# Optimization experiments

Measured on AMD Instinct MI355X. Metric: run time of the kernel, lower is better.

## Reference

```python
import jax, jax.numpy as jnp
import numpy as np

B, T, K, D = 32, 512, 4, 256
E, M = 100000, 2048
NEG = -10000000000.0


def setup_inputs() -> dict:
    key = jax.random.key(0)
    ks = jax.random.split(key, 8)
    token_reprs = jax.random.normal(ks[0], (B, T, K, D), dtype=jnp.float32)
    edge_index = jax.random.randint(ks[1], (2, E), 0, B * T, dtype=jnp.int64)
    lm_indices = jax.random.randint(ks[2], (M,), 0, B * T * K, dtype=jnp.int64)
    batch_pointers = jax.random.randint(ks[3], (M,), 0, B, dtype=jnp.int64)
    tree_padding_mask = jax.random.bernoulli(ks[4], 0.8, (B, T))
    # SwiGLU(2*dim, 4*dim, 1) parameters (no biases)
    sg = 1.0 / np.sqrt(2 * D)
    sh = 1.0 / np.sqrt(4 * D)
    Wg = jax.random.normal(ks[5], (2 * D, 4 * D), dtype=jnp.float32) * sg
    Wv = jax.random.normal(ks[6], (2 * D, 4 * D), dtype=jnp.float32) * sg
    Wo = jax.random.normal(ks[7], (4 * D, 1), dtype=jnp.float32) * sh
    return {
        "token_reprs": token_reprs,
        "Wg": Wg,
        "Wv": Wv,
        "Wo": Wo,
        "edge_index": edge_index,
        "lm_indices": lm_indices,
        "batch_pointers": batch_pointers,
        "tree_padding_mask": tree_padding_mask,
    }


def reference(token_reprs, Wg, Wv, Wo, edge_index, lm_indices, batch_pointers, tree_padding_mask):
    b, t, k, d = token_reprs.shape
    # predict_lemmas: gather type reprs via edge_index, concat, SwiGLU MLP
    type_flat = token_reprs[:, :, 0].reshape(b * t, d)           # [B*T, D]
    scope_ids, goal_ids = edge_index[0], edge_index[1]
    x = jnp.concatenate([type_flat[scope_ids], type_flat[goal_ids]], axis=-1)  # [E, 2D]
    h = jax.nn.silu(x @ Wg) * (x @ Wv)                           # [E, 4D]
    lemmas = (h @ Wo).squeeze(-1)                                # [E]
    # predict_masks: gathers + masked dot-product scoring
    mask_reprs = token_reprs.reshape(-1, d)[lm_indices]          # [M, D]
    type_reprs = token_reprs[:, :, 0]                            # [B, T, D]
    candidates = type_reprs[batch_pointers]                      # [M, T, D]
    candidate_mask = tree_padding_mask[batch_pointers]           # [M, T]
    lm_preds = jnp.einsum('md,mtd->mt', mask_reprs, candidates)  # [M, T]
    lm_preds = jnp.where(candidate_mask, lm_preds, NEG)
    return lemmas, lm_preds
```

## Files before the change

### kernel.cpp

```cpp
#include <hip/hip_runtime.h>
#include <hip/hip_bf16.h>

typedef __bf16 bf16x8 __attribute__((ext_vector_type(8)));
typedef int   i32x8 __attribute__((ext_vector_type(8)));
typedef float f32x4 __attribute__((ext_vector_type(4)));

#define KDIM 512
#define NDIM 1024
#define DDIM 256
#define TDIM 512
#define MDIM 2048
#define NROWS 16384
#define NEGV -1e10f
#define NLM 128

__device__ __forceinline__ unsigned short f2b(float f) {
    unsigned int u = __builtin_bit_cast(unsigned int, f);
    u += 0x7fffu + ((u >> 16) & 1u);
    return (unsigned short)(u >> 16);
}

typedef const __attribute__((address_space(1))) unsigned int* gas_p;
typedef __attribute__((address_space(3))) unsigned int* las_p;
__device__ __forceinline__ void gl2lds16(const void* g, void* l) {
    __builtin_amdgcn_global_load_lds((gas_p)g, (las_p)l, 16, 0, 0);
}

__global__ void prep_all(const float* __restrict__ tok,
                         const float* __restrict__ Wg,
                         const float* __restrict__ Wv,
                         const int* __restrict__ bp,
                         unsigned short* __restrict__ tfb,
                         unsigned char* __restrict__ tf8,
                         unsigned char* __restrict__ wg8,
                         unsigned char* __restrict__ wv8,
                         int* __restrict__ counts,
                         unsigned short* __restrict__ lists) {
    const int bid = blockIdx.x;
    const int tid = threadIdx.x;
    if (bid < 4096) {
        int g = (bid * 256 + tid) * 4;
        int i = g >> 8, c = g & 255;
        float4 v = *(const float4*)(tok + (size_t)i * 1024 + c);
        tfb[g + 0] = f2b(v.x);
        tfb[g + 1] = f2b(v.y);
        tfb[g + 2] = f2b(v.z);
        tfb[g + 3] = f2b(v.w);
        unsigned int p = (unsigned int)__builtin_amdgcn_cvt_pk_fp8_f32(v.x, v.y, 0, 0);
        p = (unsigned int)__builtin_amdgcn_cvt_pk_fp8_f32(v.z, v.w, (int)p, 1);
        *(unsigned int*)(tf8 + g) = p;
    } else if (bid < 4608) {
        __shared__ float tg[32][33];
        __shared__ float tv[32][33];
        int pb = bid - 4096;
        int n0 = (pb & 31) * 32, k0 = (pb >> 5) * 32;
        {
            int kk = tid >> 3, nn = (tid & 7) * 4;
            float4 g = *(const float4*)(Wg + (size_t)(k0 + kk) * NDIM + n0 + nn);
            float4 v = *(const float4*)(Wv + (size_t)(k0 + kk) * NDIM + n0 + nn);
            tg[kk][nn] = g.x; tg[kk][nn + 1] = g.y; tg[kk][nn + 2] = g.z; tg[kk][nn + 3] = g.w;
            tv[kk][nn] = v.x; tv[kk][nn + 1] = v.y; tv[kk][nn + 2] = v.z; tv[kk][nn + 3] = v.w;
        }
        __syncthreads();
        int nn2 = tid >> 3, kk2 = (tid & 7) * 4;
        unsigned int pg = (unsigned int)__builtin_amdgcn_cvt_pk_fp8_f32(
            tg[kk2][nn2], tg[kk2 + 1][nn2], 0, 0);
        pg = (unsigned int)__builtin_amdgcn_cvt_pk_fp8_f32(
            tg[kk2 + 2][nn2], tg[kk2 + 3][nn2], (int)pg, 1);
        unsigned int pv = (unsigned int)__builtin_amdgcn_cvt_pk_fp8_f32(
            tv[kk2][nn2], tv[kk2 + 1][nn2], 0, 0);
        pv = (unsigned int)__builtin_amdgcn_cvt_pk_fp8_f32(
            tv[kk2 + 2][nn2], tv[kk2 + 3][nn2], (int)pv, 1);
        *(unsigned int*)(wg8 + (size_t)(n0 + nn2) * KDIM + k0 + kk2) = pg;
        *(unsigned int*)(wv8 + (size_t)(n0 + nn2) * KDIM + k0 + kk2) = pv;
    } else {
        __shared__ int c[32];
        if (tid < 32) c[tid] = 0;
        __syncthreads();
        for (int m = tid; m < MDIM; m += 256) {
            int b = bp[m];
            int pos = atomicAdd(&c[b], 1);
            lists[b * MDIM + pos] = (unsigned short)m;
        }
        __syncthreads();
        if (tid < 32) counts[tid] = c[tid];
    }
}

__launch_bounds__(256, 2)
__global__ void fused_main(const unsigned char* __restrict__ tf8,
                           const unsigned char* __restrict__ wg8,
                           const unsigned char* __restrict__ wv8,
                           const float* __restrict__ Wo,
                           const int* __restrict__ scope,
                           const int* __restrict__ goal,
                           float* __restrict__ outLem, int E,
                           const float* __restrict__ tok,
                           const unsigned short* __restrict__ tfb,
                           const int* __restrict__ lmi,
                           const int* __restrict__ counts,
                           const unsigned short* __restrict__ lists,
                           const int* __restrict__ tpm,
                           float* __restrict__ outP) {
    __shared__ unsigned char sA[128 * 512];
    __shared__ unsigned char sB[2 * 64 * 128];

    const int tid = threadIdx.x;
    const int lane = tid & 63;
    const int w = tid >> 6;
    const int col = lane & 15;
    const int q = lane >> 4;

    if ((int)blockIdx.x < NLM) {
        const int lb = blockIdx.x;
        const int b = lb & 31;
        const int t0 = (lb >> 5) * 128;
        const int cnt = counts[b];
        for (int mt = w * 16; mt < cnt; mt += 64) {
            int mc = mt + col;
            int aid = lists[b * MDIM + (mc < cnt ? mc : cnt - 1)];
            const float* arow = tok + (size_t)lmi[aid] * DDIM;
            bf16x8 af[8];
#pragma unroll
            for (int k = 0; k < 8; k++) {
                float4 lo = *(const float4*)(arow + k * 32 + q * 8);
                float4 hi = *(const float4*)(arow + k * 32 + q * 8 + 4);
                uint4 p;
                p.x = f2b(lo.x) | ((unsigned int)f2b(lo.y) << 16);
                p.y = f2b(lo.z) | ((unsigned int)f2b(lo.w) << 16);
                p.z = f2b(hi.x) | ((unsigned int)f2b(hi.y) << 16);
                p.w = f2b(hi.z) | ((unsigned int)f2b(hi.w) << 16);
                af[k] = __builtin_bit_cast(bf16x8, p);
            }
            int gm[4];
#pragma unroll
            for (int r = 0; r < 4; r++) {
                int mrow = mt + q * 4 + r;
                gm[r] = (mrow < cnt) ? (int)lists[b * MDIM + mrow] : -1;
            }
#pragma unroll
            for (int ntile = 0; ntile < 8; ntile++) {
                int t = t0 + ntile * 16 + col;
                const unsigned short* brow = tfb + (size_t)(b * TDIM + t) * DDIM;
                f32x4 acc = (f32x4){0.f, 0.f, 0.f, 0.f};
#pragma unroll
                for (int k = 0; k < 8; k++) {
                    bf16x8 bf = __builtin_bit_cast(bf16x8,
                        *(const uint4*)(brow + k * 32 + q * 8));
                    acc = __builtin_amdgcn_mfma_f32_16x16x32_bf16(af[k], bf, acc, 0, 0, 0);
                }
                int pmv = tpm[b * TDIM + t];
#pragma unroll
                for (int r = 0; r < 4; r++) {
                    if (gm[r] >= 0)
                        outP[(size_t)gm[r] * TDIM + t] = pmv ? acc[r] : NEGV;
                }
            }
        }
        return;
    }

    const int bx = blockIdx.x - NLM;
    const int etile = bx * 128;
    const int wm = w & 1;
    const int wn = w >> 1;

#pragma unroll
    for (int i = 0; i < 16; i++) {
        int s0 = i * 16 + w * 4;
        int seg = s0 + (lane >> 4);
        int row = seg >> 1;
        int h = seg & 1;
        int e = etile + row;
        int id = (e < E) ? (h ? goal[e] : scope[e]) : 0;
        int u = lane & 15;
        int usw = (u & 8) | ((u & 7) ^ (row & 7));
        gl2lds16(tf8 + (size_t)id * DDIM + usw * 16, &sA[s0 * 256]);
    }

    float lem[16];
#pragma unroll
    for (int i = 0; i < 16; i++) lem[i] = 0.f;

    for (int nt = 0; nt < 16; nt++) {
        const int n0 = nt * 64;
        f32x4 accG[4][2], accV[4][2];
#pragma unroll
        for (int mi = 0; mi < 4; mi++)
#pragma unroll
            for (int ni = 0; ni < 2; ni++) {
                accG[mi][ni] = (f32x4){0.f, 0.f, 0.f, 0.f};
                accV[mi][ni] = (f32x4){0.f, 0.f, 0.f, 0.f};
            }
#pragma unroll
        for (int kc = 0; kc < 4; kc++) {
            __syncthreads();
#pragma unroll
            for (int a = 0; a < 2; a++)
#pragma unroll
                for (int j = 0; j < 2; j++) {
                    int rowL = w * 16 + j * 8 + (lane >> 3);
                    int u7 = (lane & 7) ^ (rowL & 7);
                    const unsigned char* src = (a ? wv8 : wg8) +
                        (size_t)(n0 + rowL) * KDIM + kc * 128 + u7 * 16;
                    gl2lds16(src, &sB[a * 8192 + (w * 16 + j * 8) * 128]);
                }
            __syncthreads();
            i32x8 af[4];
#pragma unroll
            for (int mi = 0; mi < 4; mi++) {
                int row = wm * 64 + mi * 16 + col;
                int r7 = row & 7;
                const unsigned char* base = &sA[row * 512 + (kc >> 1) * 256 + (kc & 1) * 128];
                uint4 lo = *(const uint4*)(base + (((2 * q) ^ r7) * 16));
                uint4 hi = *(const uint4*)(base + (((2 * q + 1) ^ r7) * 16));
                af[mi] = (i32x8){(int)lo.x, (int)lo.y, (int)lo.z, (int)lo.w,
                                 (int)hi.x, (int)hi.y, (int)hi.z, (int)hi.w};
            }
#pragma unroll
            for (int ni = 0; ni < 2; ni++) {
                int nl = wn * 32 + ni * 16 + col;
                int r7 = nl & 7;
                const unsigned char* bgp = &sB[nl * 128];
                uint4 lo = *(const uint4*)(bgp + (((2 * q) ^ r7) * 16));
                uint4 hi = *(const uint4*)(bgp + (((2 * q + 1) ^ r7) * 16));
                i32x8 bg = (i32x8){(int)lo.x, (int)lo.y, (int)lo.z, (int)lo.w,
                                   (int)hi.x, (int)hi.y, (int)hi.z, (int)hi.w};
                lo = *(const uint4*)(bgp + 8192 + (((2 * q) ^ r7) * 16));
                hi = *(const uint4*)(bgp + 8192 + (((2 * q + 1) ^ r7) * 16));
                i32x8 bv = (i32x8){(int)lo.x, (int)lo.y, (int)lo.z, (int)lo.w,
                                   (int)hi.x, (int)hi.y, (int)hi.z, (int)hi.w};
#pragma unroll
                for (int mi = 0; mi < 4; mi++) {
                    accG[mi][ni] = __builtin_amdgcn_mfma_scale_f32_16x16x128_f8f6f4(
                        af[mi], bg, accG[mi][ni], 0, 0, 0, 0x7F7F7F7F, 0, 0x7F7F7F7F);
                    accV[mi][ni] = __builtin_amdgcn_mfma_scale_f32_16x16x128_f8f6f4(
                        af[mi], bv, accV[mi][ni], 0, 0, 0, 0x7F7F7F7F, 0, 0x7F7F7F7F);
                }
            }
        }
#pragma unroll
        for (int ni = 0; ni < 2; ni++) {
            float wo = Wo[n0 + wn * 32 + ni * 16 + col];
#pragma unroll
            for (int mi = 0; mi < 4; mi++)
#pragma unroll
                for (int r = 0; r < 4; r++) {
                    float g = accG[mi][ni][r];
                    float v = accV[mi][ni][r];
                    float s = g / (1.f + __expf(-g));
                    lem[mi * 4 + r] += s * v * wo;
                }
        }
    }
    __syncthreads();
    float* sRed = (float*)sB;
#pragma unroll
    for (int i = 0; i < 16; i++) {
        float v = lem[i];
        for (int off = 8; off > 0; off >>= 1) v += __shfl_xor(v, off, 16);
        if (col == 0) {
            int row = wm * 64 + (i >> 2) * 16 + q * 4 + (i & 3);
            sRed[wn * 128 + row] = v;
        }
    }
    __syncthreads();
    if (tid < 128) {
        int e = etile + tid;
        if (e < E) outLem[e] = sRed[tid] + sRed[128 + tid];
    }
}

extern "C" void kernel_launch(void* const* d_in, const int* in_sizes, int n_in,
                              void* d_out, int out_size, void* d_ws, size_t ws_size,
                              hipStream_t stream) {
    const float* tok = (const float*)d_in[0];
    const float* Wg  = (const float*)d_in[1];
    const float* Wv  = (const float*)d_in[2];
    const float* Wo  = (const float*)d_in[3];
    const int* edge = (const int*)d_in[4];
    const int* lmi  = (const int*)d_in[5];
    const int* bp   = (const int*)d_in[6];
    const int* tpm  = (const int*)d_in[7];
    const int E = in_sizes[4] / 2;
    float* out = (float*)d_out;

    unsigned short* tfb = (unsigned short*)d_ws;
    unsigned char*  tf8 = (unsigned char*)(tfb + (size_t)NROWS * DDIM);
    unsigned char*  wg8 = tf8 + (size_t)NROWS * DDIM;
    unsigned char*  wv8 = wg8 + (size_t)NDIM * KDIM;
    int* counts = (int*)(wv8 + (size_t)NDIM * KDIM);
    unsigned short* lists = (unsigned short*)(counts + 32);

    prep_all<<<dim3(4609), dim3(256), 0, stream>>>(
        tok, Wg, Wv, bp, tfb, tf8, wg8, wv8, counts, lists);
    int nLemBlocks = (E + 127) / 128;
    fused_main<<<dim3(NLM + nLemBlocks), dim3(256), 0, stream>>>(
        tf8, wg8, wv8, Wo, edge, edge + E, out, E,
        tok, tfb, lmi, counts, lists, tpm, out + E);
}
```

Baseline: 268.3 us.

## Load weight B-fragments directly from global memory instead of staging through LDS

The fp8 Wg/Wv tiles are no longer staged into shared memory with two barriers per k-chunk. Each lane now loads its MFMA B operand straight from global memory, where the weights should largely hit in L2, so the per-k-chunk __syncthreads pairs disappear. A single barrier is kept after the A gather, and LDS use drops to the A tile plus a small reduction buffer. The tradeoff is redundant global loads of the same weight fragments by the two wm wave groups, more VGPRs spent holding loads, and global latency with no software prefetch.

```diff
diff --git a/kernel.cpp b/kernel.cpp
--- a/kernel.cpp
+++ b/kernel.cpp
@@ -103,7 +103,7 @@
                            const int* __restrict__ tpm,
                            float* __restrict__ outP) {
     __shared__ unsigned char sA[128 * 512];
-    __shared__ unsigned char sB[2 * 64 * 128];
+    __shared__ float sRed[256];
 
     const int tid = threadIdx.x;
     const int lane = tid & 63;
@@ -177,13 +177,18 @@
         int usw = (u & 8) | ((u & 7) ^ (row & 7));
         gl2lds16(tf8 + (size_t)id * DDIM + usw * 16, &sA[s0 * 256]);
     }
+    __syncthreads();
 
     float lem[16];
 #pragma unroll
     for (int i = 0; i < 16; i++) lem[i] = 0.f;
+
+    const unsigned char* bgbase = wg8 + (size_t)(wn * 32 + col) * KDIM + q * 32;
+    const unsigned char* bvbase = wv8 + (size_t)(wn * 32 + col) * KDIM + q * 32;
 
     for (int nt = 0; nt < 16; nt++) {
         const int n0 = nt * 64;
+        const size_t nOff = (size_t)n0 * KDIM;
         f32x4 accG[4][2], accV[4][2];
 #pragma unroll
         for (int mi = 0; mi < 4; mi++)
@@ -194,18 +199,16 @@
             }
 #pragma unroll
         for (int kc = 0; kc < 4; kc++) {
-            __syncthreads();
-#pragma unroll
-            for (int a = 0; a < 2; a++)
-#pragma unroll
-                for (int j = 0; j < 2; j++) {
-                    int rowL = w * 16 + j * 8 + (lane >> 3);
-                    int u7 = (lane & 7) ^ (rowL & 7);
-                    const unsigned char* src = (a ? wv8 : wg8) +
-                        (size_t)(n0 + rowL) * KDIM + kc * 128 + u7 * 16;
-                    gl2lds16(src, &sB[a * 8192 + (w * 16 + j * 8) * 128]);
-                }
-            __syncthreads();
+            uint4 glo[2], ghi[2], vlo[2], vhi[2];
+#pragma unroll
+            for (int ni = 0; ni < 2; ni++) {
+                const unsigned char* pg = bgbase + nOff + (size_t)ni * 16 * KDIM + kc * 128;
+                const unsigned char* pv = bvbase + nOff + (size_t)ni * 16 * KDIM + kc * 128;
+                glo[ni] = *(const uint4*)pg;
+                ghi[ni] = *(const uint4*)(pg + 16);
+                vlo[ni] = *(const uint4*)pv;
+                vhi[ni] = *(const uint4*)(pv + 16);
+            }
             i32x8 af[4];
 #pragma unroll
             for (int mi = 0; mi < 4; mi++) {
@@ -219,17 +222,10 @@
             }
 #pragma unroll
             for (int ni = 0; ni < 2; ni++) {
-                int nl = wn * 32 + ni * 16 + col;
-                int r7 = nl & 7;
-                const unsigned char* bgp = &sB[nl * 128];
-                uint4 lo = *(const uint4*)(bgp + (((2 * q) ^ r7) * 16));
-                uint4 hi = *(const uint4*)(bgp + (((2 * q + 1) ^ r7) * 16));
-                i32x8 bg = (i32x8){(int)lo.x, (int)lo.y, (int)lo.z, (int)lo.w,
-                                   (int)hi.x, (int)hi.y, (int)hi.z, (int)hi.w};
-                lo = *(const uint4*)(bgp + 8192 + (((2 * q) ^ r7) * 16));
-                hi = *(const uint4*)(bgp + 8192 + (((2 * q + 1) ^ r7) * 16));
-                i32x8 bv = (i32x8){(int)lo.x, (int)lo.y, (int)lo.z, (int)lo.w,
-                                   (int)hi.x, (int)hi.y, (int)hi.z, (int)hi.w};
+                i32x8 bg = (i32x8){(int)glo[ni].x, (int)glo[ni].y, (int)glo[ni].z, (int)glo[ni].w,
+                                   (int)ghi[ni].x, (int)ghi[ni].y, (int)ghi[ni].z, (int)ghi[ni].w};
+                i32x8 bv = (i32x8){(int)vlo[ni].x, (int)vlo[ni].y, (int)vlo[ni].z, (int)vlo[ni].w,
+                                   (int)vhi[ni].x, (int)vhi[ni].y, (int)vhi[ni].z, (int)vhi[ni].w};
 #pragma unroll
                 for (int mi = 0; mi < 4; mi++) {
                     accG[mi][ni] = __builtin_amdgcn_mfma_scale_f32_16x16x128_f8f6f4(
@@ -253,8 +249,6 @@
                 }
         }
     }
-    __syncthreads();
-    float* sRed = (float*)sB;
 #pragma unroll
     for (int i = 0; i < 16; i++) {
         float v = lem[i];
```

New measurement: 398.7 us. 1.49x slower.
